# Performance work log

Measured on AMD Instinct MI355X. Metric: run time of the kernel, lower is better.

Reference implementation:

```python
import jax, jax.numpy as jnp
import numpy as np

N_NODES = 50000
N_EDGES = 300000
INPUT_DIM = 128
HIDDEN_DIM = 256
NUM_HEADS = 8
HEAD_DIM = HIDDEN_DIM // NUM_HEADS  # 32
NUM_EDGE_TYPES = 3


def setup_inputs() -> dict:
    key = jax.random.key(0)
    ks = jax.random.split(key, 12)
    s_in = 1.0 / np.sqrt(INPUT_DIM)
    s_hid = 1.0 / np.sqrt(HIDDEN_DIM)
    return {
        "node_features": jax.random.normal(ks[0], (N_NODES, INPUT_DIM), jnp.float32),
        "edges": jax.random.randint(ks[1], (N_EDGES, 2), 0, N_NODES),
        "edge_types": jax.random.randint(ks[2], (N_EDGES,), 0, NUM_EDGE_TYPES),
        # torch.nn.Linear convention: y = x @ W.T + b, W: [out, in]
        "Wq": jax.random.normal(ks[3], (HIDDEN_DIM, INPUT_DIM), jnp.float32) * s_in,
        "bq": jax.random.normal(ks[4], (HIDDEN_DIM,), jnp.float32) * s_in,
        "Wk": jax.random.normal(ks[5], (HIDDEN_DIM, INPUT_DIM), jnp.float32) * s_in,
        "bk": jax.random.normal(ks[6], (HIDDEN_DIM,), jnp.float32) * s_in,
        "Wv": jax.random.normal(ks[7], (HIDDEN_DIM, INPUT_DIM), jnp.float32) * s_in,
        "bv": jax.random.normal(ks[8], (HIDDEN_DIM,), jnp.float32) * s_in,
        "edge_emb": jax.random.normal(ks[9], (NUM_EDGE_TYPES, HIDDEN_DIM), jnp.float32),
        "Wo": jax.random.normal(ks[10], (INPUT_DIM, HIDDEN_DIM), jnp.float32) * s_hid,
        "bo": jax.random.normal(ks[11], (INPUT_DIM,), jnp.float32) * s_hid,
    }


def reference(node_features, edges, edge_types, Wq, bq, Wk, bk, Wv, bv, edge_emb, Wo, bo):
    # Project all nodes once, split heads: [N, H, D]
    Q = (node_features @ Wq.T + bq).reshape(-1, NUM_HEADS, HEAD_DIM)
    K = (node_features @ Wk.T + bk).reshape(-1, NUM_HEADS, HEAD_DIM)
    V = (node_features @ Wv.T + bv).reshape(-1, NUM_HEADS, HEAD_DIM)

    src = edges[:, 0]
    tgt = edges[:, 1]

    # Per-edge small attention: Q[src] [E,H,D] x K[tgt]^T -> [E,H,H]
    # (identical math to the original per-edge-type loop, since only the
    #  edge embedding depends on edge_type and it is gathered per edge)
    scale = 1.0 / jnp.sqrt(jnp.float32(HEAD_DIM))
    scores = jnp.einsum("ehd,egd->ehg", Q[src], K[tgt]) * scale
    attn = jax.nn.softmax(scores, axis=-1)
    msg = jnp.einsum("ehg,egd->ehd", attn, V[tgt]).reshape(-1, HIDDEN_DIM)  # [E, HID]

    msg = msg + edge_emb[edge_types]          # per-edge-type embedding add
    out_e = msg @ Wo.T + bo                   # output projection per edge [E, IN]

    # Scatter-add over source nodes (original Python loop over edges)
    messages = jax.ops.segment_sum(out_e, src, num_segments=N_NODES)
    return messages
```

## Files before the change

kernel.cpp:

```cpp
#include <hip/hip_runtime.h>
#include <hip/hip_bf16.h>

#define N_NODES 50000
#define N_EDGES 300000
#define M_PAD 50048
#define M_PAD2 50176
#define NBLK 196
#define SC 0.17677669529663687f

#define MB_CONV 6250
#define MB_HIST 1172
#define MB_PREP 513

#define QKV_BLOCKS 782
#define SCAT_BLOCKS 586

typedef __attribute__((ext_vector_type(8))) short bf16x8;
typedef __attribute__((ext_vector_type(4))) short bf16x4;
typedef __attribute__((ext_vector_type(4))) float f32x4;

typedef __attribute__((address_space(3))) unsigned int lds_uint;
typedef const __attribute__((address_space(1))) unsigned int glb_uint;
__device__ __forceinline__ void gld16(const void* g, void* l) {
    __builtin_amdgcn_global_load_lds((glb_uint*)g, (lds_uint*)l, 16, 0, 0);
}

__device__ __forceinline__ unsigned short f2bf(float x) {
    unsigned int u = __float_as_uint(x);
    unsigned int r = (u + 0x7FFFu + ((u >> 16) & 1u)) >> 16;
    return (unsigned short)r;
}
__device__ __forceinline__ short bfs(float x) {
    __hip_bfloat16 h = __float2bfloat16(x);
    return *reinterpret_cast<short*>(&h);
}

__global__ __launch_bounds__(512)
void qkv_gemm(const unsigned short* __restrict__ A2, const unsigned short* __restrict__ B2,
              const float* __restrict__ biasCat,
              unsigned short* __restrict__ Qb, unsigned short* __restrict__ Kb,
              unsigned short* __restrict__ Vb,
              const int* __restrict__ edges, int* __restrict__ cursor,
              int* __restrict__ packed)
{
    __shared__ unsigned short A_s[64 * 128];
    __shared__ unsigned short C_s[64 * 128];
    const int bid = blockIdx.x;
    const int t   = threadIdx.x;

    if (bid >= QKV_BLOCKS) {
        const int e = (bid - QKV_BLOCKS) * 512 + t;
        if (e < N_EDGES) {
            const int pos = atomicAdd(&cursor[edges[2 * e]], 1);
            packed[pos] = edges[2 * e + 1];
        }
        return;
    }

    const int w    = t >> 6;
    const int lane = t & 63;
    const int l15  = lane & 15;
    const int lg   = lane >> 4;
    const int m0   = bid * 64;
    const int wn   = w * 16;

    {
        const char* srcbase = (const char*)A2 + (size_t)m0 * 256;
        gld16(srcbase + t * 16,              (char*)A_s + t * 16);
        gld16(srcbase + (512 + t) * 16,      (char*)A_s + (512 + t) * 16);
    }
    __syncthreads();

    #pragma unroll
    for (int mt = 0; mt < 6; ++mt) {
        const int mat = mt >> 1;
        const int nh  = mt & 1;
        const float mulc = (mat == 0) ? SC : 1.0f;
        const float bvn  = biasCat[mat * 256 + nh * 128 + wn + l15];
        const unsigned short* Bbase =
            B2 + (size_t)(mat * 256 + nh * 128 + wn + l15) * 128 + lg * 8;

        f32x4 acc[4] = {};
        #pragma unroll
        for (int ks = 0; ks < 4; ++ks) {
            const bf16x8 bfv = *(const bf16x8*)(Bbase + ks * 32);
            #pragma unroll
            for (int mi = 0; mi < 4; ++mi) {
                const int r    = mi * 16 + l15;
                const int slot = (ks * 4 + lg) ^ ((r & 7) << 1);
                const bf16x8 af = *(const bf16x8*)((const char*)A_s + r * 256 + slot * 16);
                acc[mi] = __builtin_amdgcn_mfma_f32_16x16x32_bf16(af, bfv, acc[mi], 0, 0, 0);
            }
        }

        __syncthreads();

        #pragma unroll
        for (int mi = 0; mi < 4; ++mi)
            #pragma unroll
            for (int j = 0; j < 4; ++j) {
                const int row = mi * 16 + lg * 4 + j;
                const int xr  = (row & 7) << 3;
                const int col = wn + l15;
                C_s[row * 128 + (col ^ xr)] = f2bf(fmaf(acc[mi][j], mulc, bvn));
            }
        __syncthreads();

        if (mat < 2) {
            unsigned short* dst = mat ? Kb : Qb;
            #pragma unroll
            for (int c8 = 0; c8 < 2; ++c8) {
                const int chunk = c8 * 512 + t;
                const int row = chunk >> 4;
                const int ec  = (chunk & 15) * 8;
                const bf16x8 v = *(const bf16x8*)&C_s[row * 128 + (ec ^ ((row & 7) << 3))];
                *(bf16x8*)&dst[(size_t)(m0 + row) * 256 + nh * 128 + ec] = v;
            }
        } else {
            #pragma unroll
            for (int c8 = 0; c8 < 2; ++c8) {
                const int item = c8 * 512 + t;
                const int row  = item >> 4;
                const int dlow = item & 15;
                const int xr   = (row & 7) << 3;
                bf16x8 v;
                #pragma unroll
                for (int jp = 0; jp < 8; ++jp) {
                    const int dhi = jp >> 2, gp = jp & 3;
                    const int cp  = gp * 32 + dlow + 16 * dhi;
                    v[jp] = (short)C_s[row * 128 + (cp ^ xr)];
                }
                *(bf16x8*)&Vb[(size_t)(m0 + row) * 256 + nh * 128 + dlow * 8] = v;
            }
        }
    }
}

__global__ __launch_bounds__(128)
void out_gemm(const unsigned short* __restrict__ accQ, const unsigned short* __restrict__ B2o,
              const float* __restrict__ eew, const float* __restrict__ bo,
              const float4* __restrict__ cnt4, float* __restrict__ Cout)
{
    const int t    = threadIdx.x;
    const int w    = t >> 6;
    const int lane = t & 63;
    const int l15  = lane & 15;
    const int lg   = lane >> 4;
    const int m0   = blockIdx.y * 32;
    const int wn   = w * 64;

    f32x4 acc[2][4] = {};

    const unsigned short* Abase = accQ + (size_t)(m0 + l15) * 256 + lg * 8;
    const unsigned short* Bbase = B2o + (size_t)(wn + l15) * 256 + lg * 8;

    #pragma unroll 2
    for (int ks = 0; ks < 8; ++ks) {
        bf16x8 af[2], bfv[4];
        #pragma unroll
        for (int mi = 0; mi < 2; ++mi)
            af[mi] = *(const bf16x8*)(Abase + (size_t)mi * 16 * 256 + ks * 32);
        #pragma unroll
        for (int ni = 0; ni < 4; ++ni)
            bfv[ni] = *(const bf16x8*)(Bbase + (size_t)ni * 16 * 256 + ks * 32);
        #pragma unroll
        for (int mi = 0; mi < 2; ++mi)
            #pragma unroll
            for (int ni = 0; ni < 4; ++ni)
                acc[mi][ni] = __builtin_amdgcn_mfma_f32_16x16x32_bf16(
                    af[mi], bfv[ni], acc[mi][ni], 0, 0, 0);
    }

    #pragma unroll
    for (int mi = 0; mi < 2; ++mi)
        #pragma unroll
        for (int j = 0; j < 4; ++j) {
            const int row = m0 + mi * 16 + lg * 4 + j;
            if (row < N_NODES) {
                const float4 cv = cnt4[row];
                #pragma unroll
                for (int ni = 0; ni < 4; ++ni) {
                    const int col = wn + ni * 16 + l15;
                    Cout[(size_t)row * 128 + col] = acc[mi][ni][j]
                        + cv.x * eew[col] + cv.y * eew[128 + col]
                        + cv.z * eew[256 + col] + cv.w * bo[col];
                }
            }
        }
}

__global__ __launch_bounds__(256)
void mega_prep(const float4* __restrict__ nf4,
               const int* __restrict__ edges, const int* __restrict__ etypes,
               const float* __restrict__ Wq, const float* __restrict__ Wk,
               const float* __restrict__ Wv, const float* __restrict__ bq,
               const float* __restrict__ bk, const float* __restrict__ bv,
               const float* __restrict__ Wo, const float* __restrict__ ee,
               unsigned short* __restrict__ A2, unsigned short* __restrict__ B2qkv,
               unsigned short* __restrict__ B2o,
               float* __restrict__ biasCat, float* __restrict__ eew,
               int* __restrict__ degType)
{
    const int bid = blockIdx.x, t = threadIdx.x;
    if (bid < MB_CONV) {
        const int tid = bid * 256 + t;
        const int m = tid >> 5, k4 = (tid & 31) * 4;
        const float4 v = nf4[tid];
        ushort4 hi;
        hi.x = f2bf(v.x); hi.y = f2bf(v.y); hi.z = f2bf(v.z); hi.w = f2bf(v.w);
        const int chunk = k4 >> 3;
        const int sub   = k4 & 7;
        const int scol  = ((chunk ^ ((m & 7) << 1)) << 3) + sub;
        *reinterpret_cast<ushort4*>(&A2[(size_t)m * 128 + scol]) = hi;
    } else if (bid < MB_CONV + MB_HIST) {
        const int e = (bid - MB_CONV) * 256 + t;
        if (e < N_EDGES) atomicAdd(&degType[edges[2 * e] * 4 + etypes[e]], 1);
    } else {
        const int pbid = bid - MB_CONV - MB_HIST;
        if (pbid < 384) {
            const int tid = pbid * 256 + t;
            const int r = tid >> 7, k = tid & 127;
            const float* W = (r < 256) ? Wq : (r < 512) ? Wk : Wv;
            B2qkv[(size_t)r * 128 + k] = f2bf(W[(size_t)(r & 255) * 128 + k]);
            if (k == 0) {
                const float* b = (r < 256) ? bq : (r < 512) ? bk : bv;
                biasCat[r] = b[r & 255] * ((r < 256) ? SC : 1.0f);
            }
        } else if (pbid < 512) {
            const int tid = (pbid - 384) * 256 + t;
            const int r = tid >> 8, k = tid & 255;
            B2o[(size_t)r * 256 + k] = f2bf(Wo[(size_t)r * 256 + k]);
        } else if (t < 128) {
            float a0 = 0.f, a1 = 0.f, a2 = 0.f;
            for (int k = 0; k < 256; ++k) {
                const float w = Wo[(size_t)t * 256 + k];
                a0 += ee[k] * w; a1 += ee[256 + k] * w; a2 += ee[512 + k] * w;
            }
            eew[t] = a0; eew[128 + t] = a1; eew[256 + t] = a2;
        }
    }
}

__global__ __launch_bounds__(256)
void scan_part1(const int4* __restrict__ degType4, int* __restrict__ blockSum)
{
    const int t = threadIdx.x;
    const int i = blockIdx.x * 256 + t;
    int v = 0;
    if (i < N_NODES) {
        const int4 dt = degType4[i];
        v = dt.x + dt.y + dt.z;
    }
    #pragma unroll
    for (int o = 1; o < 64; o <<= 1) v += __shfl_xor(v, o);
    __shared__ int ws[4];
    if ((t & 63) == 0) ws[t >> 6] = v;
    __syncthreads();
    if (t == 0) blockSum[blockIdx.x] = ws[0] + ws[1] + ws[2] + ws[3];
}

__global__ __launch_bounds__(256)
void scan_part2(const int* __restrict__ blockSum, int* __restrict__ blockBase,
                int* __restrict__ rowStart)
{
    __shared__ int lds[256];
    const int t = threadIdx.x;
    lds[t] = (t < NBLK) ? blockSum[t] : 0;
    __syncthreads();
    #pragma unroll
    for (int o = 1; o < 256; o <<= 1) {
        const int u = (t >= o) ? lds[t - o] : 0;
        __syncthreads();
        lds[t] += u;
        __syncthreads();
    }
    if (t < NBLK) blockBase[t] = (t == 0) ? 0 : lds[t - 1];
    if (t == 0) rowStart[N_NODES] = N_EDGES;
}

__global__ __launch_bounds__(256)
void scan_part3(const int4* __restrict__ degType4, const int* __restrict__ blockBase,
                int* __restrict__ rowStart, int* __restrict__ cursor,
                float4* __restrict__ cnt4)
{
    const int t = threadIdx.x;
    const int lane = t & 63, wid = t >> 6;
    const int i = blockIdx.x * 256 + t;
    int4 dt = make_int4(0, 0, 0, 0);
    if (i < N_NODES) dt = degType4[i];
    const int d = dt.x + dt.y + dt.z;
    int x = d;
    #pragma unroll
    for (int o = 1; o < 64; o <<= 1) {
        const int u = __shfl_up(x, o);
        if (lane >= o) x += u;
    }
    __shared__ int wtot[4];
    if (lane == 63) wtot[wid] = x;
    __syncthreads();
    int wo = 0;
    #pragma unroll
    for (int wi = 0; wi < 3; ++wi) wo += (wi < wid) ? wtot[wi] : 0;
    const int excl = blockBase[blockIdx.x] + wo + x - d;
    if (i < N_NODES) {
        rowStart[i] = excl;
        cursor[i]   = excl;
        cnt4[i]     = make_float4((float)dt.x, (float)dt.y, (float)dt.z, (float)d);
    }
}

__device__ __forceinline__ bf16x4 softmax_pa(f32x4 s, bool valid)
{
    const float e0 = __expf(s[0]), e1 = __expf(s[1]);
    const float e2 = __expf(s[2]), e3 = __expf(s[3]);
    float sum = e0 + e1 + e2 + e3;
    sum += __shfl_xor(sum, 16);
    const float inv = valid ? __builtin_amdgcn_rcpf(sum) : 0.0f;
    bf16x4 pa;
    pa[0] = bfs(e0 * inv);
    pa[1] = bfs(e1 * inv);
    pa[2] = bfs(e2 * inv);
    pa[3] = bfs(e3 * inv);
    return pa;
}

union v8split { bf16x8 v8; bf16x4 h[2]; };

__global__ __launch_bounds__(256)
void node_gather_kernel(const int* __restrict__ packed, const int* __restrict__ rowStart,
                        const unsigned short* __restrict__ Qb,
                        const unsigned short* __restrict__ Kb,
                        const unsigned short* __restrict__ Vb,
                        unsigned short* __restrict__ accQ)
{
    const int lane = threadIdx.x & 63;
    const int n = blockIdx.x * 4 + (threadIdx.x >> 6);
    if (n >= N_NODES) return;
    const int l15 = lane & 15;
    const int lg  = lane >> 4;

    const bf16x8 qf = *(const bf16x8*)&Qb[(size_t)n * 256 + (l15 & 7) * 32 + lg * 8];

    f32x4 cpvA0 = {0.f,0.f,0.f,0.f}, cpvA1 = {0.f,0.f,0.f,0.f};
    f32x4 cpvB0 = {0.f,0.f,0.f,0.f}, cpvB1 = {0.f,0.f,0.f,0.f};

    const int lo = rowStart[n], hi = rowStart[n + 1];
    const bool validBase = ((l15 < 8) == (lg < 2));
    const f32x4 z4 = {0.f, 0.f, 0.f, 0.f};
    const int voff = (lg & 1) * 128 + l15 * 8;
    int idx = lo;

    for (; idx + 4 <= hi; idx += 4) {
        const int t0 = packed[idx],     t1 = packed[idx + 1];
        const int t2 = packed[idx + 2], t3 = packed[idx + 3];

        const int tkA = (l15 < 8) ? t0 : t1;
        const int tkB = (l15 < 8) ? t2 : t3;
        const bf16x8 kfA = *(const bf16x8*)&Kb[(size_t)tkA * 256 + (l15 & 7) * 32 + lg * 8];
        const bf16x8 kfB = *(const bf16x8*)&Kb[(size_t)tkB * 256 + (l15 & 7) * 32 + lg * 8];

        const int tvA = (lg < 2) ? t0 : t1;
        const int tvB = (lg < 2) ? t2 : t3;
        v8split vA, vB;
        vA.v8 = *(const bf16x8*)&Vb[(size_t)tvA * 256 + voff];
        vB.v8 = *(const bf16x8*)&Vb[(size_t)tvB * 256 + voff];

        const f32x4 sA = __builtin_amdgcn_mfma_f32_16x16x32_bf16(kfA, qf, z4, 0, 0, 0);
        const f32x4 sB = __builtin_amdgcn_mfma_f32_16x16x32_bf16(kfB, qf, z4, 0, 0, 0);

        const bf16x4 paA = softmax_pa(sA, validBase);
        const bf16x4 paB = softmax_pa(sB, validBase);

        cpvA0 = __builtin_amdgcn_mfma_f32_16x16x16bf16_1k(paA, vA.h[0], cpvA0, 0, 0, 0);
        cpvA1 = __builtin_amdgcn_mfma_f32_16x16x16bf16_1k(paA, vA.h[1], cpvA1, 0, 0, 0);
        cpvB0 = __builtin_amdgcn_mfma_f32_16x16x16bf16_1k(paB, vB.h[0], cpvB0, 0, 0, 0);
        cpvB1 = __builtin_amdgcn_mfma_f32_16x16x16bf16_1k(paB, vB.h[1], cpvB1, 0, 0, 0);
    }

    for (; idx < hi; idx += 2) {
        const int  t0  = packed[idx];
        const bool dup = (idx + 1 >= hi);
        const int  t1  = dup ? t0 : packed[idx + 1];

        const int tk = (l15 < 8) ? t0 : t1;
        const bf16x8 kf = *(const bf16x8*)&Kb[(size_t)tk * 256 + (l15 & 7) * 32 + lg * 8];

        const int tv = (lg < 2) ? t0 : t1;
        v8split vA;
        vA.v8 = *(const bf16x8*)&Vb[(size_t)tv * 256 + voff];

        const f32x4 s = __builtin_amdgcn_mfma_f32_16x16x32_bf16(kf, qf, z4, 0, 0, 0);
        const bool valid = validBase && !(dup && (l15 >= 8));
        const bf16x4 pa = softmax_pa(s, valid);

        cpvA0 = __builtin_amdgcn_mfma_f32_16x16x16bf16_1k(pa, vA.h[0], cpvA0, 0, 0, 0);
        cpvA1 = __builtin_amdgcn_mfma_f32_16x16x16bf16_1k(pa, vA.h[1], cpvA1, 0, 0, 0);
    }

    f32x4 cpv0 = cpvA0 + cpvB0;
    f32x4 cpv1 = cpvA1 + cpvB1;

    #pragma unroll
    for (int j = 0; j < 4; ++j) {
        cpv0[j] += __shfl_xor(cpv0[j], 32);
        cpv1[j] += __shfl_xor(cpv1[j], 32);
    }

    if (lane < 32) {
        unsigned short* row = &accQ[(size_t)n * 256];
        #pragma unroll
        for (int j = 0; j < 4; ++j) {
            const int h = lg * 4 + j;
            row[h * 32 + l15]      = (unsigned short)bfs(cpv0[j]);
            row[h * 32 + 16 + l15] = (unsigned short)bfs(cpv1[j]);
        }
    }
}

extern "C" void kernel_launch(void* const* d_in, const int* in_sizes, int n_in,
                              void* d_out, int out_size, void* d_ws, size_t ws_size,
                              hipStream_t stream)
{
    const float* nf      = (const float*)d_in[0];
    const int*   edges   = (const int*)d_in[1];
    const int*   etypes  = (const int*)d_in[2];
    const float* Wq      = (const float*)d_in[3];
    const float* bq      = (const float*)d_in[4];
    const float* Wk      = (const float*)d_in[5];
    const float* bk      = (const float*)d_in[6];
    const float* Wv      = (const float*)d_in[7];
    const float* bv      = (const float*)d_in[8];
    const float* ee      = (const float*)d_in[9];
    const float* Wo      = (const float*)d_in[10];
    const float* bo      = (const float*)d_in[11];
    float* out = (float*)d_out;

    char* ws = (char*)d_ws;
    size_t off = 0;
    auto alloc = [&](size_t bytes) -> void* {
        void* p = ws + off;
        off = (off + bytes + 255) & ~(size_t)255;
        return p;
    };
    unsigned short* A2     = (unsigned short*)alloc((size_t)M_PAD * 128 * 2);
    unsigned short* B2qkv  = (unsigned short*)alloc((size_t)768 * 128 * 2);
    unsigned short* B2o    = (unsigned short*)alloc((size_t)128 * 256 * 2);
    float*          biasC  = (float*)alloc(768 * sizeof(float));
    float*          eew    = (float*)alloc(384 * sizeof(float));
    unsigned short* Qb     = (unsigned short*)alloc((size_t)M_PAD * 256 * 2);
    unsigned short* Kb     = (unsigned short*)alloc((size_t)M_PAD * 256 * 2);
    unsigned short* Vb     = (unsigned short*)alloc((size_t)M_PAD * 256 * 2);
    unsigned short* accQ   = (unsigned short*)alloc((size_t)M_PAD2 * 256 * 2);
    float4* cnt4    = (float4*)alloc((size_t)N_NODES * sizeof(float4));
    int*    degType = (int*)alloc((size_t)N_NODES * 4 * sizeof(int));
    int*    rowS    = (int*)alloc((size_t)(N_NODES + 1) * sizeof(int));
    int*    curs    = (int*)alloc((size_t)N_NODES * sizeof(int));
    int*    pck     = (int*)alloc((size_t)N_EDGES * sizeof(int));
    int*    bSum    = (int*)alloc((size_t)NBLK * sizeof(int));
    int*    bBase   = (int*)alloc((size_t)NBLK * sizeof(int));

    const dim3 blk(256);

    hipMemsetAsync(degType, 0, (size_t)N_NODES * 4 * sizeof(int), stream);
    mega_prep<<<dim3(MB_CONV + MB_HIST + MB_PREP), blk, 0, stream>>>(
        (const float4*)nf, edges, etypes, Wq, Wk, Wv, bq, bk, bv, Wo, ee,
        A2, B2qkv, B2o, biasC, eew, degType);

    scan_part1<<<dim3(NBLK), blk, 0, stream>>>((const int4*)degType, bSum);
    scan_part2<<<dim3(1), blk, 0, stream>>>(bSum, bBase, rowS);
    scan_part3<<<dim3(NBLK), blk, 0, stream>>>((const int4*)degType, bBase, rowS, curs, cnt4);

    qkv_gemm<<<dim3(QKV_BLOCKS + SCAT_BLOCKS), dim3(512), 0, stream>>>(
        A2, B2qkv, biasC, Qb, Kb, Vb, edges, curs, pck);

    node_gather_kernel<<<dim3((N_NODES + 3) / 4), blk, 0, stream>>>(
        pck, rowS, Qb, Kb, Vb, accQ);

    out_gemm<<<dim3(1, M_PAD2 / 32), dim3(128), 0, stream>>>(
        accQ, B2o, eew, bo, cnt4, out);
}
```

Measured before the change: 162.7 us.

## Split QKV GEMM across blocks per output tile with 128-row node tiles

Each block of the QKV projection kernel used to loop over all six 128-column output tiles for 64 rows. Now each block handles a 128-row tile and a single output tile, so there are six times as many blocks. Q and K results are written directly from registers with the weights as the MFMA A operand, skipping the LDS staging pass. V still goes through LDS for its permuted layout. The aim is more parallelism and less serialized work per block, at the cost of re-reading each node tile six times from global memory. A 128-row tile over 50000 nodes may also read past the padded input (391 tiles x 128 = 50048 rows), which depends on M_PAD.

```diff
diff --git a/kernel.cpp b/kernel.cpp
--- a/kernel.cpp
+++ b/kernel.cpp
@@ -12,7 +12,7 @@
 #define MB_HIST 1172
 #define MB_PREP 513
 
-#define QKV_BLOCKS 782
+#define QKV_BLOCKS 2346
 #define SCAT_BLOCKS 586
 
 typedef __attribute__((ext_vector_type(8))) short bf16x8;
@@ -43,8 +43,7 @@
               const int* __restrict__ edges, int* __restrict__ cursor,
               int* __restrict__ packed)
 {
-    __shared__ unsigned short A_s[64 * 128];
-    __shared__ unsigned short C_s[64 * 128];
+    __shared__ unsigned short A_s[128 * 128];
     const int bid = blockIdx.x;
     const int t   = threadIdx.x;
 
@@ -61,77 +60,130 @@
     const int lane = t & 63;
     const int l15  = lane & 15;
     const int lg   = lane >> 4;
-    const int m0   = bid * 64;
-    const int wn   = w * 16;
+    const int mt   = bid % 6;
+    const int mat  = mt % 3;
+    const int ch   = mt / 3;
+    const int m0   = (bid / 6) * 128;
 
     {
         const char* srcbase = (const char*)A2 + (size_t)m0 * 256;
-        gld16(srcbase + t * 16,              (char*)A_s + t * 16);
-        gld16(srcbase + (512 + t) * 16,      (char*)A_s + (512 + t) * 16);
+        #pragma unroll
+        for (int i = 0; i < 4; ++i) {
+            const int cb = (i * 8 + w) * 1024;
+            gld16(srcbase + cb + lane * 16, (char*)A_s + cb);
+        }
     }
     __syncthreads();
 
-    #pragma unroll
-    for (int mt = 0; mt < 6; ++mt) {
-        const int mat = mt >> 1;
-        const int nh  = mt & 1;
+    if (mat < 2) {
+        const int wc  = (w & 1) * 64;
+        const int wmm = (w >> 1) * 32;
+        f32x4 acc[4][2] = {};
+
+        const unsigned short* Wbase =
+            B2 + (size_t)(mat * 256 + ch * 128 + wc + l15) * 128 + lg * 8;
+
+        #pragma unroll
+        for (int ks = 0; ks < 4; ++ks) {
+            bf16x8 wf[4], nff[2];
+            #pragma unroll
+            for (int ci = 0; ci < 4; ++ci)
+                wf[ci] = *(const bf16x8*)(Wbase + (size_t)ci * 16 * 128 + ks * 32);
+            #pragma unroll
+            for (int mi = 0; mi < 2; ++mi) {
+                const int r    = wmm + mi * 16 + l15;
+                const int slot = (ks * 4 + lg) ^ ((r & 7) << 1);
+                nff[mi] = *(const bf16x8*)((const char*)A_s + r * 256 + slot * 16);
+            }
+            #pragma unroll
+            for (int ci = 0; ci < 4; ++ci)
+                #pragma unroll
+                for (int mi = 0; mi < 2; ++mi)
+                    acc[ci][mi] = __builtin_amdgcn_mfma_f32_16x16x32_bf16(
+                        wf[ci], nff[mi], acc[ci][mi], 0, 0, 0);
+        }
+
+        unsigned short* dst = mat ? Kb : Qb;
         const float mulc = (mat == 0) ? SC : 1.0f;
-        const float bvn  = biasCat[mat * 256 + nh * 128 + wn + l15];
-        const unsigned short* Bbase =
-            B2 + (size_t)(mat * 256 + nh * 128 + wn + l15) * 128 + lg * 8;
-
-        f32x4 acc[4] = {};
+        #pragma unroll
+        for (int ci = 0; ci < 4; ++ci) {
+            const int c0 = ch * 128 + wc + ci * 16 + lg * 4;
+            const float4 b4 = *(const float4*)&biasCat[mat * 256 + c0];
+            #pragma unroll
+            for (int mi = 0; mi < 2; ++mi) {
+                const int m = m0 + wmm + mi * 16 + l15;
+                ushort4 o;
+                o.x = (unsigned short)bfs(fmaf(acc[ci][mi][0], mulc, b4.x));
+                o.y = (unsigned short)bfs(fmaf(acc[ci][mi][1], mulc, b4.y));
+                o.z = (unsigned short)bfs(fmaf(acc[ci][mi][2], mulc, b4.z));
+                o.w = (unsigned short)bfs(fmaf(acc[ci][mi][3], mulc, b4.w));
+                *(ushort4*)&dst[(size_t)m * 256 + c0] = o;
+            }
+        }
+    } else {
+        const int wm = (w >> 2) * 64;
+        const int wn = (w & 3) * 32;
+        f32x4 acc[4][2] = {};
+
+        const unsigned short* Wbase =
+            B2 + (size_t)(512 + ch * 128 + wn + l15) * 128 + lg * 8;
+
         #pragma unroll
         for (int ks = 0; ks < 4; ++ks) {
-            const bf16x8 bfv = *(const bf16x8*)(Bbase + ks * 32);
+            bf16x8 nff[4], wf[2];
+            #pragma unroll
+            for (int ni = 0; ni < 2; ++ni)
+                wf[ni] = *(const bf16x8*)(Wbase + (size_t)ni * 16 * 128 + ks * 32);
             #pragma unroll
             for (int mi = 0; mi < 4; ++mi) {
-                const int r    = mi * 16 + l15;
+                const int r    = wm + mi * 16 + l15;
                 const int slot = (ks * 4 + lg) ^ ((r & 7) << 1);
-                const bf16x8 af = *(const bf16x8*)((const char*)A_s + r * 256 + slot * 16);
-                acc[mi] = __builtin_amdgcn_mfma_f32_16x16x32_bf16(af, bfv, acc[mi], 0, 0, 0);
-            }
-        }
+                nff[mi] = *(const bf16x8*)((const char*)A_s + r * 256 + slot * 16);
+            }
+            #pragma unroll
+            for (int mi = 0; mi < 4; ++mi)
+                #pragma unroll
+                for (int ni = 0; ni < 2; ++ni)
+                    acc[mi][ni] = __builtin_amdgcn_mfma_f32_16x16x32_bf16(
+                        nff[mi], wf[ni], acc[mi][ni], 0, 0, 0);
+        }
+
+        float bvn[2];
+        #pragma unroll
+        for (int ni = 0; ni < 2; ++ni)
+            bvn[ni] = biasCat[512 + ch * 128 + wn + ni * 16 + l15];
 
         __syncthreads();
+        unsigned short* C_s = A_s;
 
         #pragma unroll
         for (int mi = 0; mi < 4; ++mi)
             #pragma unroll
             for (int j = 0; j < 4; ++j) {
-                const int row = mi * 16 + lg * 4 + j;
+                const int row = wm + mi * 16 + lg * 4 + j;
                 const int xr  = (row & 7) << 3;
-                const int col = wn + l15;
-                C_s[row * 128 + (col ^ xr)] = f2bf(fmaf(acc[mi][j], mulc, bvn));
+                #pragma unroll
+                for (int ni = 0; ni < 2; ++ni) {
+                    const int col = wn + ni * 16 + l15;
+                    C_s[row * 128 + (col ^ xr)] = (unsigned short)bfs(acc[mi][ni][j] + bvn[ni]);
+                }
             }
         __syncthreads();
 
-        if (mat < 2) {
-            unsigned short* dst = mat ? Kb : Qb;
-            #pragma unroll
-            for (int c8 = 0; c8 < 2; ++c8) {
-                const int chunk = c8 * 512 + t;
-                const int row = chunk >> 4;
-                const int ec  = (chunk & 15) * 8;
-                const bf16x8 v = *(const bf16x8*)&C_s[row * 128 + (ec ^ ((row & 7) << 3))];
-                *(bf16x8*)&dst[(size_t)(m0 + row) * 256 + nh * 128 + ec] = v;
-            }
-        } else {
-            #pragma unroll
-            for (int c8 = 0; c8 < 2; ++c8) {
-                const int item = c8 * 512 + t;
-                const int row  = item >> 4;
-                const int dlow = item & 15;
-                const int xr   = (row & 7) << 3;
-                bf16x8 v;
-                #pragma unroll
-                for (int jp = 0; jp < 8; ++jp) {
-                    const int dhi = jp >> 2, gp = jp & 3;
-                    const int cp  = gp * 32 + dlow + 16 * dhi;
-                    v[jp] = (short)C_s[row * 128 + (cp ^ xr)];
-                }
-                *(bf16x8*)&Vb[(size_t)(m0 + row) * 256 + nh * 128 + dlow * 8] = v;
-            }
+        #pragma unroll
+        for (int i4 = 0; i4 < 4; ++i4) {
+            const int item = i4 * 512 + t;
+            const int row  = item >> 4;
+            const int dlow = item & 15;
+            const int xr   = (row & 7) << 3;
+            bf16x8 v;
+            #pragma unroll
+            for (int jp = 0; jp < 8; ++jp) {
+                const int dhi = jp >> 2, gp = jp & 3;
+                const int cp  = gp * 32 + dlow + 16 * dhi;
+                v[jp] = (short)C_s[row * 128 + (cp ^ xr)];
+            }
+            *(bf16x8*)&Vb[(size_t)(m0 + row) * 256 + ch * 128 + dlow * 8] = v;
         }
     }
 }
```

New measurement: 173.3 us. 1.07x slower.
